# Performance work log

Measured on AMD Instinct MI355X. Metric: run time of the kernel, lower is better.

## Reference

```python
import jax, jax.numpy as jnp
import numpy as np

B, L, D, H, K, F, M = 4, 384, 512, 8, 64, 2048, 512
NL, NCT, ND = 2, 6, 15
BINS = jnp.arange(10, 150, 10, dtype=jnp.float32)  # 14 boundaries -> 15 buckets
EPS = 1e-5


def _ln(x, g, b):
    mu = x.mean(-1, keepdims=True)
    v = ((x - mu) ** 2).mean(-1, keepdims=True)
    return (x - mu) / jnp.sqrt(v + EPS) * g + b


def _attn(x, didx, dr, mask, de, Wq, bq, Wk, bk, Wv, bv, Wo, bo):
    # x: [B,L,D]; didx: [B,L,L] distance bucket ids; dr: [B,L] dist-to-responder ids
    Q = (x @ Wq + bq).reshape(B, L, H, K)
    Kh = (x @ Wk + bk).reshape(B, L, H, K)
    V = (x @ Wv + bv).reshape(B, L, H, K)
    # NOTE: original module computes sqrt_K but never divides by it (faithful).
    E = jnp.einsum('blhk,bxhk->bhlx', Q, Kh)
    E = E + jnp.einsum('blhk,blxk->bhlx', Q, de[0][didx])          # Kqk term
    E = E + jnp.einsum('blhk,blk->bhl', Q, de[1][dr])[..., None]    # Kqr term (const over keys)
    E = E + jnp.einsum('blhk,bxk->bhlx', Q, de[2][dr])              # Kkr term
    # faithful replication of torch's mask.repeat(1,H,1,L).reshape(B,H,L,L)
    mask4 = jnp.tile(mask[None, None, :, :], (1, H, 1, L)).reshape(B, H, L, L)
    E = jnp.where(mask4 == 0, -jnp.inf, E)
    A = jax.nn.softmax(E, axis=-1)                                  # [B,H,L,L]
    Z = jnp.einsum('bhlx,bxhk->blhk', A, V)
    Z = Z + jnp.einsum('bhlx,blxk->blhk', A, de[3][didx])           # Vqk term
    Z = Z + de[4][dr][:, :, None, :]                                 # Vqr term (broadcast over heads)
    Z = Z + jnp.einsum('bhlx,bxk->blhk', A, de[5][dr])              # Vkr term
    return Z.reshape(B, L, D) @ Wo + bo


def _forward(cell_types_BL, distances_BLL, padding_mask_BL, cell_emb, dist_emb,
             Wq, bq, Wk, bk, Wv, bv, Wo, bo, W1, b1, W2, b2,
             g1, be1, g2, be2, Wm1, bm1, Wm2, bm2):
    h = cell_emb[cell_types_BL]                                      # [B,L,D]
    # torch.bucketize(right=False) == searchsorted side='left'
    didx = jnp.searchsorted(BINS, distances_BLL, side='left')        # [B,L,L]
    dr = didx[:, 0]                                                  # RESPONDER_CELL_IDX = 0
    for l in range(NL):
        a = _attn(h, didx, dr, padding_mask_BL, dist_emb,
                  Wq[l], bq[l], Wk[l], bk[l], Wv[l], bv[l], Wo[l], bo[l])
        h = _ln(h + a, g1[l], be1[l])                                # post-norm
        ff = jax.nn.gelu(h @ W1[l] + b1[l], approximate=False) @ W2[l] + b2[l]
        h = _ln(h + ff, g2[l], be2[l])
    pooled = jnp.einsum('bld,bl->bd', h, padding_mask_BL)            # mask-weighted sum pool
    return jax.nn.relu(pooled @ Wm1 + bm1) @ Wm2 + bm2               # [B,1]


def setup_inputs() -> dict:
    key = jax.random.key(0)
    ks = list(jax.random.split(key, 32))
    it = iter(ks)

    def nrm(shape, scale=0.02):
        return jax.random.normal(next(it), shape, dtype=jnp.float32) * scale

    return {
        'cell_types_BL': jax.random.randint(next(it), (B, L), 0, NCT),
        'distances_BLL': jax.random.uniform(next(it), (B, L, L), dtype=jnp.float32) * 160.0,
        'padding_mask_BL': jnp.ones((B, L), dtype=jnp.float32),
        'cell_emb': nrm((NCT, D), 1.0),
        'dist_emb': nrm((6, ND, K), 1.0),  # order: Kqk,Kqr,Kkr,Vqk,Vqr,Vkr
        'Wq': nrm((NL, D, D)), 'bq': jnp.zeros((NL, D)),
        'Wk': nrm((NL, D, D)), 'bk': jnp.zeros((NL, D)),
        'Wv': nrm((NL, D, D)), 'bv': jnp.zeros((NL, D)),
        'Wo': nrm((NL, D, D)), 'bo': jnp.zeros((NL, D)),
        'W1': nrm((NL, D, F)), 'b1': jnp.zeros((NL, F)),
        'W2': nrm((NL, F, D)), 'b2': jnp.zeros((NL, D)),
        'g1': jnp.ones((NL, D)), 'be1': jnp.zeros((NL, D)),
        'g2': jnp.ones((NL, D)), 'be2': jnp.zeros((NL, D)),
        'Wm1': nrm((D, M)), 'bm1': jnp.zeros((M,)),
        'Wm2': nrm((M, 1)), 'bm2': jnp.zeros((1,)),
    }


def reference(cell_types_BL, distances_BLL, padding_mask_BL, cell_emb, dist_emb,
              Wq, bq, Wk, bk, Wv, bv, Wo, bo, W1, b1, W2, b2,
              g1, be1, g2, be2, Wm1, bm1, Wm2, bm2):
    return _forward(cell_types_BL, distances_BLL, padding_mask_BL, cell_emb, dist_emb,
                    Wq, bq, Wk, bk, Wv, bv, Wo, bo, W1, b1, W2, b2,
                    g1, be1, g2, be2, Wm1, bm1, Wm2, bm2)
```

## Files before the change

kernel.cpp:

```cpp
#include <hip/hip_runtime.h>
#include <math.h>

#define Bb 4
#define Lq 384
#define Dm 512
#define Hh 8
#define Kk 64
#define Ff 2048
#define Mm 512
#define NLAY 2
#define NDb 15
#define BL (Bb*Lq)
#define QKVLD 1536
#define KeROWS 448
#define EP 460
#define PPs 920
#define LWP 17
#define QR 16

typedef __attribute__((ext_vector_type(8))) short bfrag;
typedef __attribute__((ext_vector_type(4))) float f32x4;
typedef __attribute__((ext_vector_type(4))) short short4v;
typedef __attribute__((ext_vector_type(2))) unsigned int uint2v;
typedef unsigned int uint;
typedef unsigned char uchar;

__device__ __forceinline__ short f2b(float f) {
    unsigned u = __builtin_bit_cast(unsigned, f);
    unsigned r = (u + 0x7fffu + ((u >> 16) & 1u)) >> 16;
    return (short)r;
}
__device__ __forceinline__ float b2f(short s) {
    unsigned u = ((unsigned)(unsigned short)s) << 16;
    return __builtin_bit_cast(float, u);
}

__device__ __forceinline__ void tile_tr(const float* __restrict__ src, short* __restrict__ dst,
                                        int Kd, int N, int t, int tx, int ty) {
    __shared__ float ts[32][33];
    int nt = t % (N / 32), kt = t / (N / 32);
    int n0 = nt * 32, k0 = kt * 32;
    for (int i = ty; i < 32; i += 8) ts[i][tx] = src[(size_t)(k0 + i) * N + n0 + tx];
    __syncthreads();
    for (int i = ty; i < 32; i += 8) dst[(size_t)(n0 + i) * Kd + k0 + tx] = f2b(ts[tx][i]);
}

__global__ __launch_bounds__(256) void prologue_all(
        const int* __restrict__ ct, const float* __restrict__ cell_emb,
        const float* __restrict__ dist, const float* __restrict__ de,
        const float* __restrict__ bq, const float* __restrict__ bk, const float* __restrict__ bv,
        const float* __restrict__ Wq, const float* __restrict__ Wk,
        const float* __restrict__ Wv, const float* __restrict__ Wo,
        const float* __restrict__ W1, const float* __restrict__ W2,
        const float* __restrict__ Wm1,
        float* __restrict__ h, short* __restrict__ hb,
        uchar* __restrict__ didx8, int* __restrict__ dr, float* __restrict__ qkvb,
        short* __restrict__ Ke, short* __restrict__ Wt_all, short* __restrict__ Wm1T) {
    const size_t WLAY = 4ull * Dm * Dm + (size_t)Dm * Ff + (size_t)Ff * Dm;
    int blk = blockIdx.x, tid = threadIdx.x;
    if (blk < 576) {
        int i = blk * 256 + tid;
        f32x4 d = *(const f32x4*)(dist + (size_t)i * 4);
        uint r = 0;
#pragma unroll
        for (int c = 0; c < 4; ++c) {
            int cnt = 0;
#pragma unroll
            for (int q = 1; q <= 14; ++q) cnt += (float)(10 * q) < d[c] ? 1 : 0;
            r |= (uint)cnt << (8 * c);
        }
        ((uint*)didx8)[i] = r;
    } else if (blk < 582) {
        int i = (blk - 576) * 256 + tid;
        if (i < BL) {
            int b = i / Lq, x = i % Lq;
            float d = dist[(size_t)b * Lq * Lq + x];
            int c = 0;
#pragma unroll
            for (int q = 1; q <= 14; ++q) c += (float)(10 * q) < d ? 1 : 0;
            dr[i] = c;
        }
    } else if (blk < 3654) {
        int i = (blk - 582) * 256 + tid;
        int row = i / Dm, d = i % Dm;
        float v = cell_emb[ct[row] * Dm + d];
        h[i] = v;
        hb[i] = f2b(v);
    } else if (blk < 3666) {
        int i = (blk - 3654) * 256 + tid;
        int l = i / QKVLD, c = i % QKVLD;
        float v = (c < Dm) ? bq[l * Dm + c] : (c < 2 * Dm) ? bk[l * Dm + c - Dm] : bv[l * Dm + c - 2 * Dm];
        qkvb[i] = v;
    } else if (blk < 4178) {
        int i = (blk - 3666) * 256 + tid;
        int k = i & 63, rr = (i >> 6) & 63, z = i >> 12;
        short v = (rr < NDb) ? f2b(de[rr * Kk + k]) : (short)0;
        Ke[((size_t)z * KeROWS + Lq + rr) * Kk + k] = v;
    } else {
        int idx = blk - 4178;
        int tx = tid & 31, ty = tid >> 5;
        if (idx < 2048) {
            int m4 = idx >> 9, rem = idx & 511, l = rem >> 8, t = rem & 255;
            const float* src = (m4 == 0 ? Wq : m4 == 1 ? Wk : m4 == 2 ? Wv : Wo) + (size_t)l * Dm * Dm;
            tile_tr(src, Wt_all + l * WLAY + (size_t)m4 * Dm * Dm, Dm, Dm, t, tx, ty);
        } else if (idx < 4096) {
            int rem = idx - 2048, l = rem >> 10, t = rem & 1023;
            tile_tr(W1 + (size_t)l * Dm * Ff, Wt_all + l * WLAY + 4ull * Dm * Dm, Dm, Ff, t, tx, ty);
        } else if (idx < 6144) {
            int rem = idx - 4096, l = rem >> 10, t = rem & 1023;
            tile_tr(W2 + (size_t)l * Ff * Dm, Wt_all + l * WLAY + 4ull * Dm * Dm + (size_t)Dm * Ff, Ff, Dm, t, tx, ty);
        } else {
            tile_tr(Wm1, Wm1T, Dm, Mm, idx - 6144, tx, ty);
        }
    }
}

__global__ __launch_bounds__(128) void qkv_gemm(const short* __restrict__ A,
                                                const short* __restrict__ Bt,
                                                const float* __restrict__ bias,
                                                const int* __restrict__ dr,
                                                const float* __restrict__ de,
                                                short* __restrict__ Qb,
                                                short* __restrict__ Ke,
                                                short* __restrict__ Vet) {
    const int tid = threadIdx.x;
    const int wave = tid >> 6, lane = tid & 63;
    const int row0 = blockIdx.y * 32, col0 = blockIdx.x * 64;
    const int r = lane & 15, g = lane >> 4;
    const int kbase = wave * (Dm / 2);
    __shared__ float red[64][33];
    f32x4 acc[2][4] = {};
#pragma unroll 4
    for (int k0 = 0; k0 < Dm / 2; k0 += 32) {
        bfrag a[2], b[4];
#pragma unroll
        for (int i = 0; i < 2; ++i)
            a[i] = *(const bfrag*)(A + (size_t)(row0 + i * 16 + r) * Dm + kbase + k0 + g * 8);
#pragma unroll
        for (int j = 0; j < 4; ++j)
            b[j] = *(const bfrag*)(Bt + (size_t)(col0 + j * 16 + r) * Dm + kbase + k0 + g * 8);
#pragma unroll
        for (int i = 0; i < 2; ++i)
#pragma unroll
            for (int j = 0; j < 4; ++j)
                acc[i][j] = __builtin_amdgcn_mfma_f32_16x16x32_bf16(a[i], b[j], acc[i][j], 0, 0, 0);
    }
    if (wave == 1) {
#pragma unroll
        for (int i = 0; i < 2; ++i)
#pragma unroll
            for (int j = 0; j < 4; ++j)
#pragma unroll
                for (int v = 0; v < 4; ++v)
                    red[lane][(i * 4 + j) * 4 + v] = acc[i][j][v];
    }
    __syncthreads();
    if (wave != 0) return;
#pragma unroll
    for (int i = 0; i < 2; ++i)
#pragma unroll
        for (int j = 0; j < 4; ++j)
#pragma unroll
            for (int v = 0; v < 4; ++v)
                acc[i][j][v] += red[lane][(i * 4 + j) * 4 + v];
    const float* de2 = de + 2 * NDb * Kk;
    const float* de5 = de + 5 * NDb * Kk;
    if (col0 < 2 * Dm) {
#pragma unroll
        for (int i = 0; i < 2; ++i)
#pragma unroll
            for (int v = 0; v < 4; ++v) {
                int row = row0 + i * 16 + g * 4 + v;
                int b = row / Lq, x = row - b * Lq;
                int dd = dr[row];
#pragma unroll
                for (int j = 0; j < 4; ++j) {
                    int col = col0 + j * 16 + r;
                    float val = acc[i][j][v] + bias[col];
                    if (col < Dm) {
                        Qb[(size_t)row * Dm + col] = f2b(val);
                    } else {
                        int k = col & 63, h2 = (col >> 6) & 7, z = b * Hh + h2;
                        Ke[((size_t)z * KeROWS + x) * Kk + k] = f2b(val + de2[dd * Kk + k]);
                    }
                }
            }
    } else {
        int h2 = (col0 >> 6) & 7;
#pragma unroll
        for (int i = 0; i < 2; ++i) {
            int rowb = row0 + i * 16 + g * 4;
            int b = rowb / Lq;
            int x0 = rowb - b * Lq;
            int z = b * Hh + h2;
            int dd[4];
#pragma unroll
            for (int v = 0; v < 4; ++v) dd[v] = dr[rowb + v];
#pragma unroll
            for (int j = 0; j < 4; ++j) {
                int k = j * 16 + r;
                float bc = bias[col0 + j * 16 + r];
                short4v pk4;
#pragma unroll
                for (int v = 0; v < 4; ++v)
                    pk4[v] = f2b(acc[i][j][v] + bc + de5[dd[v] * Kk + k]);
                *(short4v*)(Vet + ((size_t)z * Kk + k) * Lq + x0) = pk4;
            }
        }
    }
}

__global__ __launch_bounds__(256) void attn_fused(const short* __restrict__ Qb,
                                                  const short* __restrict__ Ke,
                                                  const short* __restrict__ Vet,
                                                  const uchar* __restrict__ didx8,
                                                  const int* __restrict__ dr,
                                                  const float* __restrict__ de,
                                                  short* __restrict__ Zb) {
    const int n = blockIdx.x;
    const int xcd = n & 7, kblk = n >> 3;
    const int z = xcd * 4 + (kblk & 3);
    const int qt = kblk >> 2;
    const int b = z >> 3, hh = z & 7;
    const int tid = threadIdx.x;
    const int wave = tid >> 6, lane = tid & 63;
    const int r = lane & 15, g = lane >> 4;
    __shared__ float Ef[QR * EP];
    __shared__ float lw[QR * LWP];
    __shared__ float invrow[QR];

    const int row = tid >> 4, s16 = tid & 15;
    const int grow = qt * QR + row;
    const uchar* dxp = didx8 + ((size_t)(b * Lq + grow)) * Lq + s16 * 24;
    uint2v w0 = *(const uint2v*)(dxp);
    uint2v w1 = *(const uint2v*)(dxp + 8);
    uint2v w2 = *(const uint2v*)(dxp + 16);

    const short* Qbase = Qb + ((size_t)(b * Lq + qt * QR)) * Dm + hh * Kk;
    const short* Kbase = Ke + (size_t)z * KeROWS * Kk;
    f32x4 eacc[4][2] = {};
#pragma unroll
    for (int k0 = 0; k0 < Kk; k0 += 32) {
        bfrag a = *(const bfrag*)(Qbase + (size_t)r * Dm + k0 + g * 8);
#pragma unroll
        for (int t = 0; t < 4; ++t) {
            int ctile = wave + t * 4;
            if (ctile < 14) {
                bfrag bb[2];
#pragma unroll
                for (int i = 0; i < 2; ++i)
                    bb[i] = *(const bfrag*)(Kbase + (size_t)(ctile * 32 + i * 16 + r) * Kk + k0 + g * 8);
#pragma unroll
                for (int j = 0; j < 2; ++j)
                    eacc[t][j] = __builtin_amdgcn_mfma_f32_16x16x32_bf16(a, bb[j], eacc[t][j], 0, 0, 0);
            }
        }
    }
#pragma unroll
    for (int t = 0; t < 4; ++t) {
        int ctile = wave + t * 4;
        if (ctile < 14) {
#pragma unroll
            for (int j = 0; j < 2; ++j)
#pragma unroll
                for (int v = 0; v < 4; ++v)
                    Ef[(g * 4 + v) * EP + ctile * 32 + j * 16 + r] = eacc[t][j][v];
        }
    }
    __syncthreads();

    float* Er = Ef + row * EP;
    uint dxw[6] = {w0[0], w0[1], w1[0], w1[1], w2[0], w2[1]};
    float sv[24];
    float mx = -1e30f;
#pragma unroll
    for (int u = 0; u < 6; ++u) {
        f32x4 ev = *(const f32x4*)(Er + s16 * 24 + u * 4);
        uint w = dxw[u];
#pragma unroll
        for (int c = 0; c < 4; ++c) {
            int dxv = (w >> (8 * c)) & 255;
            float s = ev[c] + Er[Lq + dxv];
            sv[u * 4 + c] = s;
            mx = fmaxf(mx, s);
        }
    }
    mx = fmaxf(mx, __shfl_xor(mx, 1));
    mx = fmaxf(mx, __shfl_xor(mx, 2));
    mx = fmaxf(mx, __shfl_xor(mx, 4));
    mx = fmaxf(mx, __shfl_xor(mx, 8));
    float sum = 0.f;
    float bins[NDb];
#pragma unroll
    for (int q = 0; q < NDb; ++q) bins[q] = 0.f;
#pragma unroll
    for (int u = 0; u < 6; ++u) {
        uint w = dxw[u];
#pragma unroll
        for (int c = 0; c < 4; ++c) {
            int dxv = (w >> (8 * c)) & 255;
            float e = __expf(sv[u * 4 + c] - mx);
            sv[u * 4 + c] = e;
            sum += e;
#pragma unroll
            for (int q = 0; q < NDb; ++q) bins[q] += (dxv == q) ? e : 0.f;
        }
    }
    sum += __shfl_xor(sum, 1);
    sum += __shfl_xor(sum, 2);
    sum += __shfl_xor(sum, 4);
    sum += __shfl_xor(sum, 8);
#pragma unroll
    for (int q = 0; q < NDb; ++q) {
        bins[q] += __shfl_xor(bins[q], 1);
        bins[q] += __shfl_xor(bins[q], 2);
        bins[q] += __shfl_xor(bins[q], 4);
        bins[q] += __shfl_xor(bins[q], 8);
    }
    float inv = 1.0f / sum;
    if (s16 == 0) {
        invrow[row] = inv;
#pragma unroll
        for (int q = 0; q < NDb; ++q) lw[row * LWP + q] = bins[q];
    }
    uint pk[12];
#pragma unroll
    for (int i = 0; i < 12; ++i) {
        uint lo = (unsigned short)f2b(sv[2 * i] * inv);
        uint hi = (unsigned short)f2b(sv[2 * i + 1] * inv);
        pk[i] = lo | (hi << 16);
    }
    __syncthreads();
    uint* prow = (uint*)((short*)Ef + row * PPs + s16 * 24);
#pragma unroll
    for (int i = 0; i < 12; ++i) prow[i] = pk[i];
    __syncthreads();

    const short* Ps = (const short*)Ef;
    const short* brow = Vet + (size_t)z * Kk * Lq + (size_t)(wave * 16 + r) * Lq;
    f32x4 pacc = {};
#pragma unroll
    for (int k0 = 0; k0 < Lq; k0 += 32) {
        bfrag bb = *(const bfrag*)(brow + k0 + g * 8);
        bfrag a = *(const bfrag*)(Ps + (size_t)r * PPs + k0 + g * 8);
        pacc = __builtin_amdgcn_mfma_f32_16x16x32_bf16(a, bb, pacc, 0, 0, 0);
    }
    const float* de3 = de + 3 * NDb * Kk;
    const float* de4 = de + 4 * NDb * Kk;
    const int k = wave * 16 + r;
    float d3[NDb];
#pragma unroll
    for (int q = 0; q < NDb; ++q) d3[q] = de3[q * Kk + k];
#pragma unroll
    for (int v = 0; v < 4; ++v) {
        int lrow = g * 4 + v;
        int gr = qt * QR + lrow;
        float wsv = 0.f;
#pragma unroll
        for (int q = 0; q < NDb; ++q) wsv += lw[lrow * LWP + q] * d3[q];
        int dd = dr[b * Lq + gr];
        float val = pacc[v] + wsv * invrow[lrow] + de4[dd * Kk + k];
        Zb[((size_t)(b * Lq + gr)) * Dm + hh * Kk + k] = f2b(val);
    }
}

template <int ACT, int OUTBF, int KD, int CT, int KW>
__global__ __launch_bounds__(64 * KW) void mfma_gemm(const short* __restrict__ A,
                                                     const short* __restrict__ Bt,
                                                     const float* __restrict__ bias,
                                                     void* __restrict__ Cv,
                                                     int lda, int ldb, int ldc) {
    const int tid = threadIdx.x;
    const int wave = tid >> 6, lane = tid & 63;
    const int row0 = blockIdx.y * 32, col0 = blockIdx.x * (16 * CT);
    const int r = lane & 15, g = lane >> 4;
    const int KC = KD / KW;
    const int kbase = wave * KC;
    __shared__ float red[KW > 1 ? KW - 1 : 1][64][2 * CT * 4 + 1];
    f32x4 acc[2][CT] = {};
#pragma unroll 4
    for (int k0 = 0; k0 < KC; k0 += 32) {
        bfrag a[2], b[CT];
#pragma unroll
        for (int i = 0; i < 2; ++i)
            a[i] = *(const bfrag*)(A + (size_t)(row0 + i * 16 + r) * lda + kbase + k0 + g * 8);
#pragma unroll
        for (int j = 0; j < CT; ++j)
            b[j] = *(const bfrag*)(Bt + (size_t)(col0 + j * 16 + r) * ldb + kbase + k0 + g * 8);
#pragma unroll
        for (int i = 0; i < 2; ++i)
#pragma unroll
            for (int j = 0; j < CT; ++j)
                acc[i][j] = __builtin_amdgcn_mfma_f32_16x16x32_bf16(a[i], b[j], acc[i][j], 0, 0, 0);
    }
    if (KW > 1) {
        if (wave > 0) {
#pragma unroll
            for (int i = 0; i < 2; ++i)
#pragma unroll
                for (int j = 0; j < CT; ++j)
#pragma unroll
                    for (int v = 0; v < 4; ++v)
                        red[wave - 1][lane][(i * CT + j) * 4 + v] = acc[i][j][v];
        }
        __syncthreads();
        if (wave != 0) return;
#pragma unroll
        for (int w = 0; w < KW - 1; ++w)
#pragma unroll
            for (int i = 0; i < 2; ++i)
#pragma unroll
                for (int j = 0; j < CT; ++j)
#pragma unroll
                    for (int v = 0; v < 4; ++v)
                        acc[i][j][v] += red[w][lane][(i * CT + j) * 4 + v];
    }
#pragma unroll
    for (int i = 0; i < 2; ++i)
#pragma unroll
        for (int j = 0; j < CT; ++j)
#pragma unroll
            for (int v = 0; v < 4; ++v) {
                int row = row0 + i * 16 + g * 4 + v;
                int col = col0 + j * 16 + r;
                float val = acc[i][j][v] + bias[col];
                if (ACT == 1) val = 0.5f * val * (1.0f + erff(val * 0.7071067811865475f));
                if (OUTBF) ((short*)Cv)[(size_t)row * ldc + col] = f2b(val);
                else       ((float*)Cv)[(size_t)row * ldc + col] = val;
            }
}

__global__ __launch_bounds__(128) void add_ln_kernel(float* __restrict__ h,
                                                     short* __restrict__ hb,
                                                     const float* __restrict__ delta,
                                                     const float* __restrict__ g,
                                                     const float* __restrict__ be) {
    const int row = blockIdx.x, t = threadIdx.x;
    const int lane = t & 63, wid = t >> 6;
    __shared__ float red[4];
    f32x4 x = *(const f32x4*)(h + (size_t)row * Dm + t * 4);
    f32x4 d = *(const f32x4*)(delta + (size_t)row * Dm + t * 4);
    x = x + d;
    float s = x[0] + x[1] + x[2] + x[3];
#pragma unroll
    for (int o = 32; o >= 1; o >>= 1) s += __shfl_xor(s, o);
    if (lane == 0) red[wid] = s;
    __syncthreads();
    float mu = (red[0] + red[1]) * (1.0f / 512.0f);
    f32x4 dif;
    float vs = 0.f;
#pragma unroll
    for (int c = 0; c < 4; ++c) { dif[c] = x[c] - mu; vs += dif[c] * dif[c]; }
#pragma unroll
    for (int o = 32; o >= 1; o >>= 1) vs += __shfl_xor(vs, o);
    if (lane == 0) red[wid + 2] = vs;
    __syncthreads();
    float rstd = rsqrtf((red[2] + red[3]) * (1.0f / 512.0f) + 1e-5f);
    f32x4 gg = *(const f32x4*)(g + t * 4);
    f32x4 bb = *(const f32x4*)(be + t * 4);
    f32x4 y;
    short4v yb;
#pragma unroll
    for (int c = 0; c < 4; ++c) { y[c] = dif[c] * rstd * gg[c] + bb[c]; yb[c] = f2b(y[c]); }
    *(f32x4*)(h + (size_t)row * Dm + t * 4) = y;
    *(short4v*)(hb + (size_t)row * Dm + t * 4) = yb;
}

__global__ __launch_bounds__(512) void pool_partial(const float* __restrict__ h,
                                                    const float* __restrict__ mask,
                                                    float* __restrict__ partial) {
    int c = blockIdx.x, b = blockIdx.y, d = threadIdx.x;
    float acc = 0.f;
#pragma unroll 8
    for (int i = 0; i < 64; ++i) {
        int l = c * 64 + i;
        acc += h[((size_t)(b * Lq + l)) * Dm + d] * mask[b * Lq + l];
    }
    partial[((size_t)(b * 6 + c)) * Dm + d] = acc;
}

__global__ __launch_bounds__(256) void head_mlp(const float* __restrict__ partial,
                                                const short* __restrict__ Wm1T,
                                                const float* __restrict__ bm1,
                                                const float* __restrict__ Wm2,
                                                float* __restrict__ mlp_t) {
    int w = blockIdx.x * 4 + (threadIdx.x >> 6);
    int lane = threadIdx.x & 63;
    int m = w >> 2, b = w & 3;
    const short* wr = Wm1T + (size_t)m * Dm;
    float acc = 0.f;
#pragma unroll
    for (int i = 0; i < 8; ++i) {
        int k = lane * 8 + i;
        float pool = 0.f;
#pragma unroll
        for (int c = 0; c < 6; ++c) pool += partial[((size_t)(b * 6 + c)) * Dm + k];
        acc += pool * b2f(wr[k]);
    }
#pragma unroll
    for (int off = 32; off >= 1; off >>= 1) acc += __shfl_xor(acc, off);
    if (lane == 0) mlp_t[b * Mm + m] = fmaxf(acc + bm1[m], 0.f) * Wm2[m];
}

__global__ __launch_bounds__(256) void final_kernel(const float* __restrict__ mlp_t,
                                                    const float* __restrict__ bm2,
                                                    float* __restrict__ out) {
    int b = blockIdx.x, t = threadIdx.x;
    int lane = t & 63, wid = t >> 6;
    __shared__ float red[4];
    float v = mlp_t[b * Mm + t] + mlp_t[b * Mm + 256 + t];
#pragma unroll
    for (int off = 32; off >= 1; off >>= 1) v += __shfl_xor(v, off);
    if (lane == 0) red[wid] = v;
    __syncthreads();
    if (t == 0) out[b] = red[0] + red[1] + red[2] + red[3] + bm2[0];
}

extern "C" void kernel_launch(void* const* d_in, const int* in_sizes, int n_in,
                              void* d_out, int out_size, void* d_ws, size_t ws_size,
                              hipStream_t stream) {
    const int* ct        = (const int*)d_in[0];
    const float* dist    = (const float*)d_in[1];
    const float* mask    = (const float*)d_in[2];
    const float* cellemb = (const float*)d_in[3];
    const float* de      = (const float*)d_in[4];
    const float* Wq = (const float*)d_in[5];
    const float* bq = (const float*)d_in[6];
    const float* Wk = (const float*)d_in[7];
    const float* bk = (const float*)d_in[8];
    const float* Wv = (const float*)d_in[9];
    const float* bv = (const float*)d_in[10];
    const float* Wo = (const float*)d_in[11];
    const float* bo = (const float*)d_in[12];
    const float* W1 = (const float*)d_in[13];
    const float* b1 = (const float*)d_in[14];
    const float* W2 = (const float*)d_in[15];
    const float* b2 = (const float*)d_in[16];
    const float* g1 = (const float*)d_in[17];
    const float* be1 = (const float*)d_in[18];
    const float* g2 = (const float*)d_in[19];
    const float* be2 = (const float*)d_in[20];
    const float* Wm1 = (const float*)d_in[21];
    const float* bm1 = (const float*)d_in[22];
    const float* Wm2 = (const float*)d_in[23];
    const float* bm2 = (const float*)d_in[24];
    float* out = (float*)d_out;

    float* ws = (float*)d_ws;
    float* h       = ws;
    float* tmp     = h + (size_t)BL * Dm;
    float* qkvb    = tmp + (size_t)BL * Dm;
    float* partial = qkvb + NLAY * QKVLD;
    float* mlp_t   = partial + (size_t)Bb * 6 * Dm;
    int* dr        = (int*)(mlp_t + Bb * Mm);
    uchar* didx8   = (uchar*)(dr + Bb * Lq);
    short* hb      = (short*)(didx8 + (size_t)Bb * Lq * Lq);
    short* Qb      = hb + (size_t)BL * Dm;
    short* Zb      = Qb + (size_t)BL * Dm;
    short* ffb     = Zb + (size_t)BL * Dm;
    short* Wt_all  = ffb + (size_t)BL * Ff;
    const size_t WLAY = 4ull * Dm * Dm + (size_t)Dm * Ff + (size_t)Ff * Dm;
    short* Wm1T    = Wt_all + NLAY * WLAY;
    short* Ke      = Wm1T + (size_t)Mm * Dm;
    short* Vet     = Ke + (size_t)Bb * Hh * KeROWS * Kk;

    prologue_all<<<10578, 256, 0, stream>>>(ct, cellemb, dist, de, bq, bk, bv,
                                            Wq, Wk, Wv, Wo, W1, W2, Wm1,
                                            h, hb, didx8, dr, qkvb, Ke, Wt_all, Wm1T);

    dim3 gQKV(QKVLD / 64, BL / 32);
    dim3 gD(Dm / 32, BL / 32);
    dim3 gF(Ff / 64, BL / 32);

    for (int l = 0; l < NLAY; ++l) {
        short* base = Wt_all + l * WLAY;
        short* WoT = base + 3 * Dm * Dm;
        short* W1T = base + 4 * Dm * Dm;
        short* W2T = base + 4 * Dm * Dm + Dm * Ff;

        qkv_gemm<<<gQKV, 128, 0, stream>>>(hb, base, qkvb + l * QKVLD, dr, de, Qb, Ke, Vet);
        attn_fused<<<768, 256, 0, stream>>>(Qb, Ke, Vet, didx8, dr, de, Zb);

        mfma_gemm<0, 0, Dm, 2, 2><<<gD, 128, 0, stream>>>(Zb, WoT, bo + l * Dm, tmp, Dm, Dm, Dm);
        add_ln_kernel<<<BL, 128, 0, stream>>>(h, hb, tmp, g1 + l * Dm, be1 + l * Dm);

        mfma_gemm<1, 1, Dm, 4, 2><<<gF, 128, 0, stream>>>(hb, W1T, b1 + l * Ff, ffb, Dm, Dm, Ff);
        mfma_gemm<0, 0, Ff, 2, 4><<<gD, 256, 0, stream>>>(ffb, W2T, b2 + l * Dm, tmp, Ff, Ff, Dm);
        add_ln_kernel<<<BL, 128, 0, stream>>>(h, hb, tmp, g2 + l * Dm, be2 + l * Dm);
    }

    pool_partial<<<dim3(6, Bb), 512, 0, stream>>>(h, mask, partial);
    head_mlp<<<512, 256, 0, stream>>>(partial, Wm1T, bm1, Wm2, mlp_t);
    final_kernel<<<Bb, 256, 0, stream>>>(mlp_t, bm2, out);
}
```

Measured before the change: 236.1 us.

## Double attention block threads and split PV reduction across two wave halves

The attention kernel now launches with 512 threads instead of 256. Each row's softmax is spread over 32 threads instead of 16, and the score MFMA tiles are spread across 8 waves. The P·V product is split along the key dimension between two groups of four waves, and the partial sums are combined through shared memory. This is meant to cut per-thread serial work and latency for this small-grid kernel, at the cost of an extra barrier, more shuffles and lower occupancy per CU.

New measurement: 234.2 us (median of 2 runs). Within noise of the previous version (-0.8%).

```diff
diff --git a/kernel.cpp b/kernel.cpp
--- a/kernel.cpp
+++ b/kernel.cpp
@@ -210,7 +210,7 @@
     }
 }
 
-__global__ __launch_bounds__(256) void attn_fused(const short* __restrict__ Qb,
+__global__ __launch_bounds__(512) void attn_fused(const short* __restrict__ Qb,
                                                   const short* __restrict__ Ke,
                                                   const short* __restrict__ Vet,
                                                   const uchar* __restrict__ didx8,
@@ -228,23 +228,24 @@
     __shared__ float Ef[QR * EP];
     __shared__ float lw[QR * LWP];
     __shared__ float invrow[QR];
-
-    const int row = tid >> 4, s16 = tid & 15;
+    __shared__ float pred[4][64][5];
+
+    const int row = tid >> 5, s32 = tid & 31;
     const int grow = qt * QR + row;
-    const uchar* dxp = didx8 + ((size_t)(b * Lq + grow)) * Lq + s16 * 24;
-    uint2v w0 = *(const uint2v*)(dxp);
-    uint2v w1 = *(const uint2v*)(dxp + 8);
-    uint2v w2 = *(const uint2v*)(dxp + 16);
+    const uchar* dxp = didx8 + ((size_t)(b * Lq + grow)) * Lq + s32 * 12;
+    uint w0 = *(const uint*)(dxp);
+    uint w1 = *(const uint*)(dxp + 4);
+    uint w2 = *(const uint*)(dxp + 8);
 
     const short* Qbase = Qb + ((size_t)(b * Lq + qt * QR)) * Dm + hh * Kk;
     const short* Kbase = Ke + (size_t)z * KeROWS * Kk;
-    f32x4 eacc[4][2] = {};
+    f32x4 eacc[2][2] = {};
 #pragma unroll
     for (int k0 = 0; k0 < Kk; k0 += 32) {
         bfrag a = *(const bfrag*)(Qbase + (size_t)r * Dm + k0 + g * 8);
 #pragma unroll
-        for (int t = 0; t < 4; ++t) {
-            int ctile = wave + t * 4;
+        for (int t = 0; t < 2; ++t) {
+            int ctile = wave + t * 8;
             if (ctile < 14) {
                 bfrag bb[2];
 #pragma unroll
@@ -257,8 +258,8 @@
         }
     }
 #pragma unroll
-    for (int t = 0; t < 4; ++t) {
-        int ctile = wave + t * 4;
+    for (int t = 0; t < 2; ++t) {
+        int ctile = wave + t * 8;
         if (ctile < 14) {
 #pragma unroll
             for (int j = 0; j < 2; ++j)
@@ -270,12 +271,12 @@
     __syncthreads();
 
     float* Er = Ef + row * EP;
-    uint dxw[6] = {w0[0], w0[1], w1[0], w1[1], w2[0], w2[1]};
-    float sv[24];
+    uint dxw[3] = {w0, w1, w2};
+    float sv[12];
     float mx = -1e30f;
 #pragma unroll
-    for (int u = 0; u < 6; ++u) {
-        f32x4 ev = *(const f32x4*)(Er + s16 * 24 + u * 4);
+    for (int u = 0; u < 3; ++u) {
+        f32x4 ev = *(const f32x4*)(Er + s32 * 12 + u * 4);
         uint w = dxw[u];
 #pragma unroll
         for (int c = 0; c < 4; ++c) {
@@ -289,12 +290,13 @@
     mx = fmaxf(mx, __shfl_xor(mx, 2));
     mx = fmaxf(mx, __shfl_xor(mx, 4));
     mx = fmaxf(mx, __shfl_xor(mx, 8));
+    mx = fmaxf(mx, __shfl_xor(mx, 16));
     float sum = 0.f;
     float bins[NDb];
 #pragma unroll
     for (int q = 0; q < NDb; ++q) bins[q] = 0.f;
 #pragma unroll
-    for (int u = 0; u < 6; ++u) {
+    for (int u = 0; u < 3; ++u) {
         uint w = dxw[u];
 #pragma unroll
         for (int c = 0; c < 4; ++c) {
@@ -310,44 +312,56 @@
     sum += __shfl_xor(sum, 2);
     sum += __shfl_xor(sum, 4);
     sum += __shfl_xor(sum, 8);
+    sum += __shfl_xor(sum, 16);
 #pragma unroll
     for (int q = 0; q < NDb; ++q) {
         bins[q] += __shfl_xor(bins[q], 1);
         bins[q] += __shfl_xor(bins[q], 2);
         bins[q] += __shfl_xor(bins[q], 4);
         bins[q] += __shfl_xor(bins[q], 8);
+        bins[q] += __shfl_xor(bins[q], 16);
     }
     float inv = 1.0f / sum;
-    if (s16 == 0) {
+    if (s32 == 0) {
         invrow[row] = inv;
 #pragma unroll
         for (int q = 0; q < NDb; ++q) lw[row * LWP + q] = bins[q];
     }
-    uint pk[12];
-#pragma unroll
-    for (int i = 0; i < 12; ++i) {
+    uint pk[6];
+#pragma unroll
+    for (int i = 0; i < 6; ++i) {
         uint lo = (unsigned short)f2b(sv[2 * i] * inv);
         uint hi = (unsigned short)f2b(sv[2 * i + 1] * inv);
         pk[i] = lo | (hi << 16);
     }
     __syncthreads();
-    uint* prow = (uint*)((short*)Ef + row * PPs + s16 * 24);
-#pragma unroll
-    for (int i = 0; i < 12; ++i) prow[i] = pk[i];
-    __syncthreads();
-
+    uint* prow = (uint*)((short*)Ef + row * PPs + s32 * 12);
+#pragma unroll
+    for (int i = 0; i < 6; ++i) prow[i] = pk[i];
+    __syncthreads();
+
+    const int half = wave >> 2, w4 = wave & 3;
     const short* Ps = (const short*)Ef;
-    const short* brow = Vet + (size_t)z * Kk * Lq + (size_t)(wave * 16 + r) * Lq;
+    const short* brow = Vet + (size_t)z * Kk * Lq + (size_t)(w4 * 16 + r) * Lq;
+    const int kv0 = half * (Lq / 2);
     f32x4 pacc = {};
 #pragma unroll
-    for (int k0 = 0; k0 < Lq; k0 += 32) {
-        bfrag bb = *(const bfrag*)(brow + k0 + g * 8);
-        bfrag a = *(const bfrag*)(Ps + (size_t)r * PPs + k0 + g * 8);
+    for (int k0 = 0; k0 < Lq / 2; k0 += 32) {
+        bfrag bb = *(const bfrag*)(brow + kv0 + k0 + g * 8);
+        bfrag a = *(const bfrag*)(Ps + (size_t)r * PPs + kv0 + k0 + g * 8);
         pacc = __builtin_amdgcn_mfma_f32_16x16x32_bf16(a, bb, pacc, 0, 0, 0);
     }
+    if (half == 1) {
+#pragma unroll
+        for (int v = 0; v < 4; ++v) pred[w4][lane][v] = pacc[v];
+    }
+    __syncthreads();
+    if (half == 1) return;
+#pragma unroll
+    for (int v = 0; v < 4; ++v) pacc[v] += pred[w4][lane][v];
     const float* de3 = de + 3 * NDb * Kk;
     const float* de4 = de + 4 * NDb * Kk;
-    const int k = wave * 16 + r;
+    const int k = w4 * 16 + r;
     float d3[NDb];
 #pragma unroll
     for (int q = 0; q < NDb; ++q) d3[q] = de3[q * Kk + k];
@@ -579,7 +593,7 @@
         short* W2T = base + 4 * Dm * Dm + Dm * Ff;
 
         qkv_gemm<<<gQKV, 128, 0, stream>>>(hb, base, qkvb + l * QKVLD, dr, de, Qb, Ke, Vet);
-        attn_fused<<<768, 256, 0, stream>>>(Qb, Ke, Vet, didx8, dr, de, Zb);
+        attn_fused<<<768, 512, 0, stream>>>(Qb, Ke, Vet, didx8, dr, de, Zb);
 
         mfma_gemm<0, 0, Dm, 2, 2><<<gD, 128, 0, stream>>>(Zb, WoT, bo + l * Dm, tmp, Dm, Dm, Dm);
         add_ln_kernel<<<BL, 128, 0, stream>>>(h, hb, tmp, g1 + l * Dm, be1 + l * Dm);
```
